# Kernel optimization log

Hardware: AMD Instinct MI355X
Metric: run time of the kernel (lower is better)

Reference implementation:

```python
import jax, jax.numpy as jnp
import numpy as np

INPUT_DIM, HIDDEN_DIM, N_HEADS, N_AGENTS = 256, 512, 8, 64
BATCH, N_ENTITIES = 128, 256


def setup_inputs() -> dict:
    key = jax.random.key(0)
    ks = jax.random.split(key, 6)
    x = jax.random.normal(ks[0], (BATCH, N_ENTITIES, INPUT_DIM), dtype=jnp.float32)
    # encode: LeakyReLU -> Linear(input_dim, hidden_dim)
    W_enc = jax.random.normal(ks[1], (INPUT_DIM, HIDDEN_DIM), dtype=jnp.float32) * (1.0 / np.sqrt(INPUT_DIM))
    b_enc = jnp.zeros((HIDDEN_DIM,), dtype=jnp.float32)
    # per-head full hidden x hidden projections, stacked on head axis
    WQ = jax.random.normal(ks[2], (N_HEADS, HIDDEN_DIM, HIDDEN_DIM), dtype=jnp.float32)
    WK = jax.random.normal(ks[3], (N_HEADS, HIDDEN_DIM, HIDDEN_DIM), dtype=jnp.float32)
    WV = jax.random.normal(ks[4], (N_HEADS, HIDDEN_DIM, HIDDEN_DIM), dtype=jnp.float32)
    return {"x": x, "W_enc": W_enc, "b_enc": b_enc, "WQ": WQ, "WK": WK, "WV": WV, "n_agents": N_AGENTS}


def reference(x, W_enc, b_enc, WQ, WK, WV, n_agents):
    scale = 1.0 / np.sqrt(WQ.shape[-1]).astype(np.float32)
    # encode: LeakyReLU(0.01) then Linear
    h = jax.nn.leaky_relu(x, negative_slope=0.01) @ W_enc + b_enc  # [b, e, H]
    ha = h[:, :n_agents]  # [b, a, H]
    # all heads at once: n = head axis
    Q = jnp.einsum('bah,nhd->nbad', ha, WQ)
    K = jnp.einsum('beh,nhd->nbed', h, WK)
    V = jnp.einsum('beh,nhd->nbed', h, WV)
    scores = jnp.einsum('nbad,nbed->nbae', Q, K) * scale
    p = jax.nn.softmax(scores, axis=-1)
    # redundant renormalization from the original code
    prob = p / (jnp.sum(p, axis=-1, keepdims=True) + 1e-12)
    z = jnp.einsum('nbae,nbed->nbad', prob, V)  # [n, b, a, H]
    return jnp.mean(z, axis=0)  # [b, a, H]
```

## Files before the change

kernel.cpp:

```cpp
#include <hip/hip_runtime.h>
#include <math.h>

#define BATCH  128
#define NENT   256
#define INDIM  256
#define HID    512
#define NHEAD  8
#define NAGENT 64
#define SCALE  0.04419417382415922f


typedef unsigned short u16;
typedef unsigned int   u32;

typedef __bf16 bf16x8  __attribute__((ext_vector_type(8)));
typedef float  floatx4 __attribute__((ext_vector_type(4)));
typedef u32    u32x4   __attribute__((ext_vector_type(4)));
typedef u32    u32x2   __attribute__((ext_vector_type(2)));

union Frag {
    u32x4 s;
    struct { u32x2 lo, hi; } p;
    bf16x8 v;
};

__device__ __forceinline__ u16 f2bf(float x) {
    u32 u = __float_as_uint(x);
    return (u16)((u + 0x7FFFu + ((u >> 16) & 1u)) >> 16);
}
__device__ __forceinline__ float bf2f(u16 b) {
    return __uint_as_float(((u32)b) << 16);
}
__device__ __forceinline__ void split4(const float4& r, ushort4& hh, ushort4& hl) {
    hh.x = f2bf(r.x); hl.x = f2bf(r.x - bf2f(hh.x));
    hh.y = f2bf(r.y); hl.y = f2bf(r.y - bf2f(hh.y));
    hh.z = f2bf(r.z); hl.z = f2bf(r.z - bf2f(hh.z));
    hh.w = f2bf(r.w); hl.w = f2bf(r.w - bf2f(hh.w));
}

__global__ __launch_bounds__(256) void wenc_t_kernel(const float* __restrict__ W,
                                                     u16* __restrict__ Wt_p) {
    __shared__ float tile[64][68];
    const int bid = blockIdx.x;
    const int k0 = (bid & 3) * 64;
    const int d0 = (bid >> 2) * 64;
    const int t = threadIdx.x;
    const int ki = t >> 2, dc = (t & 3) * 16;
    #pragma unroll
    for (int c = 0; c < 4; ++c)
        *(float4*)&tile[ki][dc + c * 4] =
            *(const float4*)(W + (size_t)(k0 + ki) * HID + d0 + dc + c * 4);
    __syncthreads();
    const int dr = t >> 2, kc = (t & 3) * 16;
    #pragma unroll
    for (int c = 0; c < 4; ++c) {
        float4 v = make_float4(tile[kc + c * 4 + 0][dr], tile[kc + c * 4 + 1][dr],
                               tile[kc + c * 4 + 2][dr], tile[kc + c * 4 + 3][dr]);
        ushort4 hh, hl; split4(v, hh, hl);
        const int kk = k0 + kc + c * 4;
        size_t o = (size_t)(d0 + dr) * 512 + (size_t)(kk >> 5) * 64 + (kk & 31);
        *(ushort4*)(Wt_p + o) = hh;
        *(ushort4*)(Wt_p + o + 32) = hl;
    }
}

__global__ __launch_bounds__(256) void enc_kernel(const float* __restrict__ x,
                                                  const u16* __restrict__ Wt_p,
                                                  const float* __restrict__ bias,
                                                  u16* __restrict__ h_p) {
    __shared__ u16 Ah[32][264];
    __shared__ u16 Al[32][264];
    const int r0 = blockIdx.x * 32;
    const int t  = threadIdx.x;
    {
        const int row = t >> 3;
        const float* xr = x + (size_t)(r0 + row) * INDIM;
        #pragma unroll
        for (int j = 0; j < 8; ++j) {
            const int k0 = ((t & 7) + j * 8) * 4;
            float4 v = *(const float4*)(xr + k0);
            v.x = v.x > 0.f ? v.x : 0.01f * v.x;
            v.y = v.y > 0.f ? v.y : 0.01f * v.y;
            v.z = v.z > 0.f ? v.z : 0.01f * v.z;
            v.w = v.w > 0.f ? v.w : 0.01f * v.w;
            ushort4 hh, hl; split4(v, hh, hl);
            *(ushort4*)&Ah[row][k0] = hh;
            *(ushort4*)&Al[row][k0] = hl;
        }
    }
    __syncthreads();

    const int wid = t >> 6, lane = t & 63, l15 = lane & 15, quad = lane >> 4;
    const int mbase = (wid & 1) * 16;
    const int nbase = (wid >> 1) * 256;
    const floatx4 z4 = {0.f, 0.f, 0.f, 0.f};
    floatx4 acc[16];
    #pragma unroll
    for (int i = 0; i < 16; ++i) acc[i] = z4;

    for (int ks = 0; ks < 8; ++ks) {
        const int k = ks * 32 + quad * 8;
        Frag Afh, Afl;
        Afh.s = *(const u32x4*)&Ah[mbase + l15][k];
        Afl.s = *(const u32x4*)&Al[mbase + l15][k];
        #pragma unroll
        for (int nt = 0; nt < 16; ++nt) {
            const int d = nbase + nt * 16 + l15;
            const size_t wo = (size_t)d * 512 + (size_t)ks * 64 + quad * 8;
            Frag Bh, Bl;
            Bh.s = *(const u32x4*)(Wt_p + wo);
            Bl.s = *(const u32x4*)(Wt_p + wo + 32);
            floatx4 c = acc[nt];
            c = __builtin_amdgcn_mfma_f32_16x16x32_bf16(Afh.v, Bh.v, c, 0, 0, 0);
            c = __builtin_amdgcn_mfma_f32_16x16x32_bf16(Afh.v, Bl.v, c, 0, 0, 0);
            c = __builtin_amdgcn_mfma_f32_16x16x32_bf16(Afl.v, Bh.v, c, 0, 0, 0);
            acc[nt] = c;
        }
    }
    #pragma unroll
    for (int nt = 0; nt < 16; ++nt) {
        const int d = nbase + nt * 16 + l15;
        const float bv = bias[d];
        #pragma unroll
        for (int r = 0; r < 4; ++r) {
            const float v = acc[nt][r] + bv;
            const u16 hi = f2bf(v);
            const u16 lo = f2bf(v - bf2f(hi));
            const size_t o = (size_t)(r0 + mbase + quad * 4 + r) * 1024
                           + (size_t)(d >> 5) * 64 + (d & 31);
            h_p[o]      = hi;
            h_p[o + 32] = lo;
        }
    }
}

__global__ __launch_bounds__(256) void ht_kernel(const u16* __restrict__ h_p,
                                                 u16* __restrict__ hT) {
    __shared__ u16 tile[64][72];
    const int bid = blockIdx.x;
    const int dt = bid & 7;
    const int et = (bid >> 3) & 3;
    const int b  = bid >> 5;
    const int t  = threadIdx.x;
    const int r  = t >> 2, cs = (t & 3) * 16;
    const int dg = dt * 64 + cs;
    const u16* src = h_p + (size_t)(b * 256 + et * 64 + r) * 1024
                   + (size_t)(dg >> 5) * 64 + (dg & 31);
    *(ushort4*)&tile[r][cs + 0]  = *(const ushort4*)(src + 0);
    *(ushort4*)&tile[r][cs + 4]  = *(const ushort4*)(src + 4);
    *(ushort4*)&tile[r][cs + 8]  = *(const ushort4*)(src + 8);
    *(ushort4*)&tile[r][cs + 12] = *(const ushort4*)(src + 12);
    __syncthreads();
    const int d = t >> 2, es = (t & 3) * 16;
    u16* dst = hT + (size_t)b * 131072 + (size_t)(dt * 64 + d) * 256 + et * 64 + es;
    #pragma unroll
    for (int c = 0; c < 4; ++c) {
        ushort4 v = make_ushort4(tile[es + c * 4 + 0][d], tile[es + c * 4 + 1][d],
                                 tile[es + c * 4 + 2][d], tile[es + c * 4 + 3][d]);
        *(ushort4*)(dst + c * 4) = v;
    }
}

__global__ __launch_bounds__(256) void wqk_kernel(const float* __restrict__ WQ,
                                                  const float* __restrict__ WK,
                                                  u16* __restrict__ Mt_p) {
    __shared__ u16 Ah[64][72], Al[64][72], Bh[64][72], Bl[64][72];
    const int bid = blockIdx.x;
    const int jt = (bid & 7) * 64;
    const int it = ((bid >> 3) & 7) * 64;
    const int n  = bid >> 6;
    const float* qp = WQ + (size_t)n * 262144;
    const float* kp = WK + (size_t)n * 262144;
    const int t = threadIdx.x;
    const int wid = t >> 6, lane = t & 63, l15 = lane & 15, quad = lane >> 4;
    const int srow = t >> 2, sc = (t & 3) * 16;

    const floatx4 z4 = {0.f, 0.f, 0.f, 0.f};
    floatx4 acc[4];
    #pragma unroll
    for (int i = 0; i < 4; ++i) acc[i] = z4;

    for (int kc = 0; kc < HID; kc += 64) {
        #pragma unroll
        for (int f = 0; f < 4; ++f) {
            float4 va = *(const float4*)(kp + (size_t)(jt + srow) * HID + kc + sc + f * 4);
            ushort4 hh, hl; split4(va, hh, hl);
            *(ushort4*)&Ah[srow][sc + f * 4] = hh;
            *(ushort4*)&Al[srow][sc + f * 4] = hl;
            float4 vb = *(const float4*)(qp + (size_t)(it + srow) * HID + kc + sc + f * 4);
            split4(vb, hh, hl);
            *(ushort4*)&Bh[srow][sc + f * 4] = hh;
            *(ushort4*)&Bl[srow][sc + f * 4] = hl;
        }
        __syncthreads();
        #pragma unroll
        for (int ks = 0; ks < 2; ++ks) {
            const int k = ks * 32 + quad * 8;
            Frag Afh, Afl;
            Afh.s = *(const u32x4*)&Ah[wid * 16 + l15][k];
            Afl.s = *(const u32x4*)&Al[wid * 16 + l15][k];
            #pragma unroll
            for (int nt = 0; nt < 4; ++nt) {
                Frag Bfh, Bfl;
                Bfh.s = *(const u32x4*)&Bh[nt * 16 + l15][k];
                Bfl.s = *(const u32x4*)&Bl[nt * 16 + l15][k];
                floatx4 c = acc[nt];
                c = __builtin_amdgcn_mfma_f32_16x16x32_bf16(Afh.v, Bfh.v, c, 0, 0, 0);
                c = __builtin_amdgcn_mfma_f32_16x16x32_bf16(Afh.v, Bfl.v, c, 0, 0, 0);
                c = __builtin_amdgcn_mfma_f32_16x16x32_bf16(Afl.v, Bfh.v, c, 0, 0, 0);
                acc[nt] = c;
            }
        }
        __syncthreads();
    }
    #pragma unroll
    for (int nt = 0; nt < 4; ++nt)
        #pragma unroll
        for (int r = 0; r < 4; ++r) {
            const float v = acc[nt][r] * SCALE;
            const u16 hi = f2bf(v);
            const u16 lo = f2bf(v - bf2f(hi));
            const int j = jt + wid * 16 + quad * 4 + r;
            const int i = it + nt * 16 + l15;
            const size_t o = (size_t)n * 524288 + (size_t)j * 1024
                           + (size_t)(i >> 5) * 64 + (i & 31);
            Mt_p[o]      = hi;
            Mt_p[o + 32] = lo;
        }
}

__global__ __launch_bounds__(256) void wvt_kernel(const float* __restrict__ WV,
                                                  u16* __restrict__ WVt) {
    __shared__ float tile[64][68];
    const int bid = blockIdx.x;
    const int i0 = (bid & 7) * 64;
    const int o0 = ((bid >> 3) & 7) * 64;
    const int n  = bid >> 6;
    const float* src = WV + (size_t)n * 262144;
    const int t  = threadIdx.x;
    const int di = t >> 2;
    const int dc = (t & 3) * 16;
    #pragma unroll
    for (int c = 0; c < 4; ++c)
        *(float4*)&tile[di][dc + c * 4] =
            *(const float4*)(src + (size_t)(i0 + di) * HID + o0 + dc + c * 4);
    __syncthreads();
    const int dr = t >> 2;
    const int ic = (t & 3) * 16;
    size_t o = (size_t)n * 262144 + (size_t)(o0 + dr) * HID + i0 + ic;
    #pragma unroll
    for (int c = 0; c < 4; ++c) {
        ushort4 v = make_ushort4(f2bf(tile[ic + c * 4 + 0][dr]), f2bf(tile[ic + c * 4 + 1][dr]),
                                 f2bf(tile[ic + c * 4 + 2][dr]), f2bf(tile[ic + c * 4 + 3][dr]));
        *(ushort4*)(WVt + o + c * 4) = v;
    }
}

template<bool USE_HT>
__global__ __launch_bounds__(256, 3) void attn_kernel(const u16* __restrict__ h_p,
                                                      const u16* __restrict__ Mt_p,
                                                      const u16* __restrict__ WVt,
                                                      const u16* __restrict__ hT,
                                                      float* __restrict__ out) {
    constexpr int SMSZ = USE_HT ? 34816 : 53504;
    __shared__ __align__(16) char SM[SMSZ];
    u16*   Th  = (u16*)SM;
    u16*   Tl  = (u16*)(SM + 16640);
    float* S   = (float*)SM;
    float* red = (float*)(SM + 33792);
    u16*   HbT = (u16*)SM;
    u16*   U   = (u16*)SM;
    u16*   Pt  = (u16*)(SM + (USE_HT ? 0 : 36864));

    const int bid = blockIdx.x;
    const int x7 = bid & 7;
    const int s  = bid >> 3;
    const int at = s & 1;
    const int n  = (x7 >> 1) | (((s >> 1) & 1) << 2);
    const int b  = ((s >> 2) << 1) | (x7 & 1);

    const int tid  = threadIdx.x;
    const int wid  = tid >> 6;
    const int lane = tid & 63;
    const int l15  = lane & 15;
    const int quad = lane >> 4;

    const u16* Mtp = Mt_p + (size_t)n * 524288;
    const u16* Wv  = WVt  + (size_t)n * 262144;
    const u16* hTb = hT + (size_t)b * 131072;
    const size_t hb_base = (size_t)b * 262144;
    const size_t ha_row0 = hb_base + (size_t)(at * 32) * 1024;

    const floatx4 z4 = {0.f, 0.f, 0.f, 0.f};
    floatx4 Sacc[8];
    #pragma unroll
    for (int i = 0; i < 8; ++i) Sacc[i] = z4;

    for (int H = 0; H < 2; ++H) {
        floatx4 Tacc[8];
        #pragma unroll
        for (int i = 0; i < 8; ++i) Tacc[i] = z4;
        for (int ks = 0; ks < 16; ++ks) {
            const int ko = ks * 64 + quad * 8;
            Frag Ahf[2], Alf[2];
            #pragma unroll
            for (int mt = 0; mt < 2; ++mt) {
                const size_t ro = ha_row0 + (size_t)(mt * 16 + l15) * 1024 + ko;
                Ahf[mt].s = *(const u32x4*)(h_p + ro);
                Alf[mt].s = *(const u32x4*)(h_p + ro + 32);
            }
            #pragma unroll
            for (int nt = 0; nt < 4; ++nt) {
                const int d = H * 256 + (wid * 4 + nt) * 16 + l15;
                const size_t mo = (size_t)d * 1024 + ko;
                Frag Bh, Bl;
                Bh.s = *(const u32x4*)(Mtp + mo);
                Bl.s = *(const u32x4*)(Mtp + mo + 32);
                #pragma unroll
                for (int mt = 0; mt < 2; ++mt) {
                    floatx4 c = Tacc[mt * 4 + nt];
                    c = __builtin_amdgcn_mfma_f32_16x16x32_bf16(Ahf[mt].v, Bh.v, c, 0, 0, 0);
                    c = __builtin_amdgcn_mfma_f32_16x16x32_bf16(Ahf[mt].v, Bl.v, c, 0, 0, 0);
                    c = __builtin_amdgcn_mfma_f32_16x16x32_bf16(Alf[mt].v, Bh.v, c, 0, 0, 0);
                    Tacc[mt * 4 + nt] = c;
                }
            }
        }
        __syncthreads();
        #pragma unroll
        for (int mt = 0; mt < 2; ++mt)
            #pragma unroll
            for (int nt = 0; nt < 4; ++nt)
                #pragma unroll
                for (int r = 0; r < 4; ++r) {
                    const float v = Tacc[mt * 4 + nt][r];
                    const int a  = mt * 16 + quad * 4 + r;
                    const int dl = (wid * 4 + nt) * 16 + l15;
                    const u16 hi = f2bf(v);
                    Th[a * 260 + dl] = hi;
                    Tl[a * 260 + dl] = f2bf(v - bf2f(hi));
                }
        __syncthreads();
        for (int ks = 0; ks < 8; ++ks) {
            const int kl = ks * 32 + quad * 8;
            const int ko = (H * 8 + ks) * 64 + quad * 8;
            Frag Ahf[4], Alf[4];
            #pragma unroll
            for (int mt = 0; mt < 4; ++mt) {
                const size_t ro = hb_base + (size_t)((wid * 4 + mt) * 16 + l15) * 1024 + ko;
                Ahf[mt].s = *(const u32x4*)(h_p + ro);
                Alf[mt].s = *(const u32x4*)(h_p + ro + 32);
            }
            #pragma unroll
            for (int nt = 0; nt < 2; ++nt) {
                const int ac = nt * 16 + l15;
                Frag Bfh, Bfl;
                Bfh.p.lo = *(const u32x2*)(Th + ac * 260 + kl);
                Bfh.p.hi = *(const u32x2*)(Th + ac * 260 + kl + 4);
                Bfl.p.lo = *(const u32x2*)(Tl + ac * 260 + kl);
                Bfl.p.hi = *(const u32x2*)(Tl + ac * 260 + kl + 4);
                #pragma unroll
                for (int mt = 0; mt < 4; ++mt) {
                    floatx4 c = Sacc[mt * 2 + nt];
                    c = __builtin_amdgcn_mfma_f32_16x16x32_bf16(Ahf[mt].v, Bfh.v, c, 0, 0, 0);
                    c = __builtin_amdgcn_mfma_f32_16x16x32_bf16(Ahf[mt].v, Bfl.v, c, 0, 0, 0);
                    c = __builtin_amdgcn_mfma_f32_16x16x32_bf16(Alf[mt].v, Bfh.v, c, 0, 0, 0);
                    Sacc[mt * 2 + nt] = c;
                }
            }
        }
    }
    __syncthreads();
    #pragma unroll
    for (int mt = 0; mt < 4; ++mt)
        #pragma unroll
        for (int nt = 0; nt < 2; ++nt)
            #pragma unroll
            for (int r = 0; r < 4; ++r) {
                const int e = (wid * 4 + mt) * 16 + quad * 4 + r;
                const int a = nt * 16 + l15;
                S[e * 33 + a] = Sacc[mt * 2 + nt][r];
            }
    __syncthreads();
    {
        const int a   = tid & 31;
        const int seg = tid >> 5;
        float v[32];
        #pragma unroll
        for (int i = 0; i < 32; ++i) v[i] = S[(seg * 32 + i) * 33 + a];
        float mx = v[0];
        #pragma unroll
        for (int i = 1; i < 32; ++i) mx = fmaxf(mx, v[i]);
        red[a * 8 + seg] = mx;
        __syncthreads();
        float gmx = red[a * 8 + 0];
        #pragma unroll
        for (int i = 1; i < 8; ++i) gmx = fmaxf(gmx, red[a * 8 + i]);
        __syncthreads();
        float sum = 0.f;
        #pragma unroll
        for (int i = 0; i < 32; ++i) { v[i] = expf(v[i] - gmx); sum += v[i]; }
        red[a * 8 + seg] = sum;
        __syncthreads();
        float tot = 0.f;
        #pragma unroll
        for (int i = 0; i < 8; ++i) tot += red[a * 8 + i];
        const float inv = 1.0f / tot;
        #pragma unroll
        for (int i = 0; i < 32; ++i)
            Pt[a * 260 + seg * 32 + i] = f2bf(v[i] * inv);
    }
    __syncthreads();
    floatx4 Uacc[16];
    #pragma unroll
    for (int i = 0; i < 16; ++i) Uacc[i] = z4;
    const int d0w = wid * 128;
    if (USE_HT) {
        for (int ep = 0; ep < 4; ++ep) {
            Frag Bc[2][8];
            #pragma unroll
            for (int sb = 0; sb < 2; ++sb)
                #pragma unroll
                for (int dt = 0; dt < 8; ++dt) {
                    const int d = d0w + dt * 16 + l15;
                    Bc[sb][dt].s = *(const u32x4*)(hTb + (size_t)d * 256
                                                   + (2 * ep + sb) * 32 + quad * 8);
                }
            #pragma unroll
            for (int sb = 0; sb < 2; ++sb) {
                const int et = 2 * ep + sb;
                Frag Ap[2];
                #pragma unroll
                for (int mt = 0; mt < 2; ++mt) {
                    const int ar = mt * 16 + l15;
                    Ap[mt].p.lo = *(const u32x2*)(Pt + ar * 260 + et * 32 + quad * 8);
                    Ap[mt].p.hi = *(const u32x2*)(Pt + ar * 260 + et * 32 + quad * 8 + 4);
                }
                #pragma unroll
                for (int dt = 0; dt < 8; ++dt)
                    #pragma unroll
                    for (int mt = 0; mt < 2; ++mt)
                        Uacc[mt * 8 + dt] = __builtin_amdgcn_mfma_f32_16x16x32_bf16(
                            Ap[mt].v, Bc[sb][dt].v, Uacc[mt * 8 + dt], 0, 0, 0);
            }
        }
    } else {
        u32* Hb32 = (u32*)HbT;
        for (int et = 0; et < 8; ++et) {
            {
                const int epi = lane & 15;
                const int q   = lane >> 4;
                const size_t r0p = hb_base + (size_t)(et * 32 + 2 * epi) * 1024;
                #pragma unroll
                for (int c = 0; c < 4; ++c) {
                    const int d0 = d0w + c * 32 + q * 8;
                    const size_t po = (size_t)(d0 >> 5) * 64 + (d0 & 31);
                    u32x4 u0 = *(const u32x4*)(h_p + r0p + po);
                    u32x4 u1 = *(const u32x4*)(h_p + r0p + 1024 + po);
                    #pragma unroll
                    for (int p = 0; p < 4; ++p) {
                        const u32 w0 = (u0[p] & 0xFFFFu) | (u1[p] << 16);
                        const u32 w1 = (u0[p] >> 16) | (u1[p] & 0xFFFF0000u);
                        Hb32[(d0 + 2 * p) * 18 + epi]     = w0;
                        Hb32[(d0 + 2 * p + 1) * 18 + epi] = w1;
                    }
                }
            }
            Frag Ap[2];
            #pragma unroll
            for (int mt = 0; mt < 2; ++mt) {
                const int ar = mt * 16 + l15;
                Ap[mt].p.lo = *(const u32x2*)(Pt + ar * 260 + et * 32 + quad * 8);
                Ap[mt].p.hi = *(const u32x2*)(Pt + ar * 260 + et * 32 + quad * 8 + 4);
            }
            #pragma unroll
            for (int dt = 0; dt < 8; ++dt) {
                const int d = d0w + dt * 16 + l15;
                Frag Bf;
                Bf.p.lo = *(const u32x2*)(HbT + d * 36 + quad * 8);
                Bf.p.hi = *(const u32x2*)(HbT + d * 36 + quad * 8 + 4);
                #pragma unroll
                for (int mt = 0; mt < 2; ++mt)
                    Uacc[mt * 8 + dt] = __builtin_amdgcn_mfma_f32_16x16x32_bf16(
                        Ap[mt].v, Bf.v, Uacc[mt * 8 + dt], 0, 0, 0);
            }
        }
    }
    __syncthreads();
    #pragma unroll
    for (int mt = 0; mt < 2; ++mt)
        #pragma unroll
        for (int dt = 0; dt < 8; ++dt)
            #pragma unroll
            for (int r = 0; r < 4; ++r) {
                const int a = mt * 16 + quad * 4 + r;
                const int d = d0w + dt * 16 + l15;
                U[a * 520 + d] = f2bf(Uacc[mt * 8 + dt][r]);
            }
    __syncthreads();
    floatx4 Zacc[16];
    #pragma unroll
    for (int i = 0; i < 16; ++i) Zacc[i] = z4;
    for (int kp = 0; kp < 8; ++kp) {
        Frag Bw[2][8];
        #pragma unroll
        for (int sb = 0; sb < 2; ++sb) {
            const int k = (kp * 2 + sb) * 32 + quad * 8;
            #pragma unroll
            for (int dt = 0; dt < 8; ++dt) {
                const int dn = (wid * 8 + dt) * 16 + l15;
                Bw[sb][dt].s = *(const u32x4*)(Wv + (size_t)dn * HID + k);
            }
        }
        #pragma unroll
        for (int sb = 0; sb < 2; ++sb) {
            const int k = (kp * 2 + sb) * 32 + quad * 8;
            Frag Au[2];
            #pragma unroll
            for (int mt = 0; mt < 2; ++mt) {
                Au[mt].p.lo = *(const u32x2*)(U + (mt * 16 + l15) * 520 + k);
                Au[mt].p.hi = *(const u32x2*)(U + (mt * 16 + l15) * 520 + k + 4);
            }
            #pragma unroll
            for (int dt = 0; dt < 8; ++dt)
                #pragma unroll
                for (int mt = 0; mt < 2; ++mt)
                    Zacc[mt * 8 + dt] = __builtin_amdgcn_mfma_f32_16x16x32_bf16(
                        Au[mt].v, Bw[sb][dt].v, Zacc[mt * 8 + dt], 0, 0, 0);
        }
    }
    float* ob = out + ((size_t)b * NAGENT + at * 32) * HID;
    #pragma unroll
    for (int mt = 0; mt < 2; ++mt)
        #pragma unroll
        for (int dt = 0; dt < 8; ++dt)
            #pragma unroll
            for (int r = 0; r < 4; ++r) {
                const int a  = mt * 16 + quad * 4 + r;
                const int dn = (wid * 8 + dt) * 16 + l15;
                atomicAdd(ob + (size_t)a * HID + dn, Zacc[mt * 8 + dt][r] * 0.125f);
            }
}

extern "C" void kernel_launch(void* const* d_in, const int* in_sizes, int n_in,
                              void* d_out, int out_size, void* d_ws, size_t ws_size,
                              hipStream_t stream) {
    const float* x     = (const float*)d_in[0];
    const float* W_enc = (const float*)d_in[1];
    const float* b_enc = (const float*)d_in[2];
    const float* WQ    = (const float*)d_in[3];
    const float* WK    = (const float*)d_in[4];
    const float* WV    = (const float*)d_in[5];
    float* out = (float*)d_out;

    char* ws = (char*)d_ws;
    u16* h_p  = (u16*)ws;
    u16* Mt_p = (u16*)(ws + 67108864);
    u16* WVt  = (u16*)(ws + 75497472);
    u16* hT   = (u16*)(ws + 79691776);
    u16* Wt_p = WVt;

    const bool useHT = ws_size >= (size_t)113246208;

    hipMemsetAsync(d_out, 0, (size_t)out_size * sizeof(float), stream);
    wenc_t_kernel<<<32, 256, 0, stream>>>(W_enc, Wt_p);
    enc_kernel<<<1024, 256, 0, stream>>>(x, Wt_p, b_enc, h_p);
    if (useHT) ht_kernel<<<4096, 256, 0, stream>>>(h_p, hT);
    wvt_kernel<<<512, 256, 0, stream>>>(WV, WVt);
    wqk_kernel<<<512, 256, 0, stream>>>(WQ, WK, Mt_p);
    if (useHT)
        attn_kernel<true><<<2048, 256, 0, stream>>>(h_p, Mt_p, WVt, hT, out);
    else
        attn_kernel<false><<<2048, 256, 0, stream>>>(h_p, Mt_p, WVt, hT, out);
}
```

Baseline: 971.0 us.

## Double-buffer global operand loads in register across all fused GEMM phases

Each GEMM stage of the fused attention kernel (T=ha·M, S=h·T, U=P·hT, Z=U·WV) now uses two register fragment sets. The loads for the next k-step are issued before the MFMAs of the current step, and the first loads of each stage are hoisted above the preceding __syncthreads. The goal is to hide global-memory latency behind matrix-core work instead of stalling at the start of each k-iteration. The cost is many more live VGPRs, which risks spills or lower occupancy. The prefetch loops also read one step past the last k-slice, into memory that is never used.

After: 961.4 us. About the same (-1.0%).

```diff
diff --git a/kernel.cpp b/kernel.cpp
--- a/kernel.cpp
+++ b/kernel.cpp
@@ -36,6 +36,9 @@
     hh.y = f2bf(r.y); hl.y = f2bf(r.y - bf2f(hh.y));
     hh.z = f2bf(r.z); hl.z = f2bf(r.z - bf2f(hh.z));
     hh.w = f2bf(r.w); hl.w = f2bf(r.w - bf2f(hh.w));
+}
+__device__ __forceinline__ floatx4 mm(const Frag& a, const Frag& b, floatx4 c) {
+    return __builtin_amdgcn_mfma_f32_16x16x32_bf16(a.v, b.v, c, 0, 0, 0);
 }
 
 __global__ __launch_bounds__(256) void wenc_t_kernel(const float* __restrict__ W,
@@ -296,36 +299,67 @@
     #pragma unroll
     for (int i = 0; i < 8; ++i) Sacc[i] = z4;
 
+    const u16* hA  = h_p + ha_row0 + (size_t)l15 * 1024 + quad * 8;
+    const u16* hB  = h_p + hb_base + (size_t)(wid * 64 + l15) * 1024 + quad * 8;
+
+#define LDA4(SET, KS) do { const u16* _p = hA + (size_t)(KS) * 64;                     \
+        SET##h0.s = *(const u32x4*)(_p);         SET##l0.s = *(const u32x4*)(_p + 32);   \
+        SET##h1.s = *(const u32x4*)(_p + 16384); SET##l1.s = *(const u32x4*)(_p + 16416);} while (0)
+#define LDB2(SET, KS, NT) do { const u16* _p = MtB + (NT) * 16384 + (size_t)(KS) * 64;  \
+        SET##h.s = *(const u32x4*)(_p);          SET##l.s = *(const u32x4*)(_p + 32); } while (0)
+#define MFA(AS, BS, NT) do {                                                            \
+        floatx4 c0 = Tacc[NT], c1 = Tacc[4 + (NT)];                                     \
+        c0 = mm(AS##h0, BS##h, c0); c0 = mm(AS##h0, BS##l, c0); c0 = mm(AS##l0, BS##h, c0); \
+        c1 = mm(AS##h1, BS##h, c1); c1 = mm(AS##h1, BS##l, c1); c1 = mm(AS##l1, BS##h, c1); \
+        Tacc[NT] = c0; Tacc[4 + (NT)] = c1; } while (0)
+#define LDP8(SET, KO) do { const u16* _p = hB + (size_t)(KO) * 64;                      \
+        SET##h0.s = *(const u32x4*)(_p);         SET##l0.s = *(const u32x4*)(_p + 32);   \
+        SET##h1.s = *(const u32x4*)(_p + 16384); SET##l1.s = *(const u32x4*)(_p + 16416);\
+        SET##h2.s = *(const u32x4*)(_p + 32768); SET##l2.s = *(const u32x4*)(_p + 32800);\
+        SET##h3.s = *(const u32x4*)(_p + 49152); SET##l3.s = *(const u32x4*)(_p + 49184);} while (0)
+#define MFMB(AS, KS) do {                                                               \
+        const int _kl = (KS) * 32 + quad * 8;                                           \
+        Frag _h0, _l0, _h1, _l1;                                                        \
+        _h0.p.lo = *(const u32x2*)(Th + l15 * 260 + _kl);                               \
+        _h0.p.hi = *(const u32x2*)(Th + l15 * 260 + _kl + 4);                           \
+        _l0.p.lo = *(const u32x2*)(Tl + l15 * 260 + _kl);                               \
+        _l0.p.hi = *(const u32x2*)(Tl + l15 * 260 + _kl + 4);                           \
+        _h1.p.lo = *(const u32x2*)(Th + (16 + l15) * 260 + _kl);                        \
+        _h1.p.hi = *(const u32x2*)(Th + (16 + l15) * 260 + _kl + 4);                    \
+        _l1.p.lo = *(const u32x2*)(Tl + (16 + l15) * 260 + _kl);                        \
+        _l1.p.hi = *(const u32x2*)(Tl + (16 + l15) * 260 + _kl + 4);                    \
+        Sacc[0] = mm(AS##h0, _h0, Sacc[0]); Sacc[0] = mm(AS##h0, _l0, Sacc[0]); Sacc[0] = mm(AS##l0, _h0, Sacc[0]); \
+        Sacc[2] = mm(AS##h1, _h0, Sacc[2]); Sacc[2] = mm(AS##h1, _l0, Sacc[2]); Sacc[2] = mm(AS##l1, _h0, Sacc[2]); \
+        Sacc[4] = mm(AS##h2, _h0, Sacc[4]); Sacc[4] = mm(AS##h2, _l0, Sacc[4]); Sacc[4] = mm(AS##l2, _h0, Sacc[4]); \
+        Sacc[6] = mm(AS##h3, _h0, Sacc[6]); Sacc[6] = mm(AS##h3, _l0, Sacc[6]); Sacc[6] = mm(AS##l3, _h0, Sacc[6]); \
+        Sacc[1] = mm(AS##h0, _h1, Sacc[1]); Sacc[1] = mm(AS##h0, _l1, Sacc[1]); Sacc[1] = mm(AS##l0, _h1, Sacc[1]); \
+        Sacc[3] = mm(AS##h1, _h1, Sacc[3]); Sacc[3] = mm(AS##h1, _l1, Sacc[3]); Sacc[3] = mm(AS##l1, _h1, Sacc[3]); \
+        Sacc[5] = mm(AS##h2, _h1, Sacc[5]); Sacc[5] = mm(AS##h2, _l1, Sacc[5]); Sacc[5] = mm(AS##l2, _h1, Sacc[5]); \
+        Sacc[7] = mm(AS##h3, _h1, Sacc[7]); Sacc[7] = mm(AS##h3, _l1, Sacc[7]); Sacc[7] = mm(AS##l3, _h1, Sacc[7]); } while (0)
+
     for (int H = 0; H < 2; ++H) {
         floatx4 Tacc[8];
         #pragma unroll
         for (int i = 0; i < 8; ++i) Tacc[i] = z4;
-        for (int ks = 0; ks < 16; ++ks) {
-            const int ko = ks * 64 + quad * 8;
-            Frag Ahf[2], Alf[2];
-            #pragma unroll
-            for (int mt = 0; mt < 2; ++mt) {
-                const size_t ro = ha_row0 + (size_t)(mt * 16 + l15) * 1024 + ko;
-                Ahf[mt].s = *(const u32x4*)(h_p + ro);
-                Alf[mt].s = *(const u32x4*)(h_p + ro + 32);
-            }
-            #pragma unroll
-            for (int nt = 0; nt < 4; ++nt) {
-                const int d = H * 256 + (wid * 4 + nt) * 16 + l15;
-                const size_t mo = (size_t)d * 1024 + ko;
-                Frag Bh, Bl;
-                Bh.s = *(const u32x4*)(Mtp + mo);
-                Bl.s = *(const u32x4*)(Mtp + mo + 32);
-                #pragma unroll
-                for (int mt = 0; mt < 2; ++mt) {
-                    floatx4 c = Tacc[mt * 4 + nt];
-                    c = __builtin_amdgcn_mfma_f32_16x16x32_bf16(Ahf[mt].v, Bh.v, c, 0, 0, 0);
-                    c = __builtin_amdgcn_mfma_f32_16x16x32_bf16(Ahf[mt].v, Bl.v, c, 0, 0, 0);
-                    c = __builtin_amdgcn_mfma_f32_16x16x32_bf16(Alf[mt].v, Bh.v, c, 0, 0, 0);
-                    Tacc[mt * 4 + nt] = c;
-                }
-            }
-        }
+        const u16* MtB = Mtp + (size_t)(H * 256 + wid * 64 + l15) * 1024 + quad * 8;
+        Frag A0h0, A0l0, A0h1, A0l1, A1h0, A1l0, A1h1, A1l1;
+        Frag B0h, B0l, B1h, B1l;
+        LDA4(A0, 0); LDB2(B0, 0, 0);
+        for (int ks = 0; ks < 16; ks += 2) {
+            LDA4(A1, ks + 1);
+            LDB2(B1, ks, 1);      MFA(A0, B0, 0);
+            LDB2(B0, ks, 2);      MFA(A0, B1, 1);
+            LDB2(B1, ks, 3);      MFA(A0, B0, 2);
+            LDB2(B0, ks + 1, 0);  MFA(A0, B1, 3);
+            LDA4(A0, ks + 2);
+            LDB2(B1, ks + 1, 1);  MFA(A1, B0, 0);
+            LDB2(B0, ks + 1, 2);  MFA(A1, B1, 1);
+            LDB2(B1, ks + 1, 3);  MFA(A1, B0, 2);
+            LDB2(B0, ks + 2, 0);  MFA(A1, B1, 3);
+        }
+        Frag P0h0, P0l0, P0h1, P0l1, P0h2, P0l2, P0h3, P0l3;
+        Frag P1h0, P1l0, P1h1, P1l1, P1h2, P1l2, P1h3, P1l3;
+        LDP8(P0, H * 8);
         __syncthreads();
         #pragma unroll
         for (int mt = 0; mt < 2; ++mt)
@@ -341,33 +375,11 @@
                     Tl[a * 260 + dl] = f2bf(v - bf2f(hi));
                 }
         __syncthreads();
-        for (int ks = 0; ks < 8; ++ks) {
-            const int kl = ks * 32 + quad * 8;
-            const int ko = (H * 8 + ks) * 64 + quad * 8;
-            Frag Ahf[4], Alf[4];
-            #pragma unroll
-            for (int mt = 0; mt < 4; ++mt) {
-                const size_t ro = hb_base + (size_t)((wid * 4 + mt) * 16 + l15) * 1024 + ko;
-                Ahf[mt].s = *(const u32x4*)(h_p + ro);
-                Alf[mt].s = *(const u32x4*)(h_p + ro + 32);
-            }
-            #pragma unroll
-            for (int nt = 0; nt < 2; ++nt) {
-                const int ac = nt * 16 + l15;
-                Frag Bfh, Bfl;
-                Bfh.p.lo = *(const u32x2*)(Th + ac * 260 + kl);
-                Bfh.p.hi = *(const u32x2*)(Th + ac * 260 + kl + 4);
-                Bfl.p.lo = *(const u32x2*)(Tl + ac * 260 + kl);
-                Bfl.p.hi = *(const u32x2*)(Tl + ac * 260 + kl + 4);
-                #pragma unroll
-                for (int mt = 0; mt < 4; ++mt) {
-                    floatx4 c = Sacc[mt * 2 + nt];
-                    c = __builtin_amdgcn_mfma_f32_16x16x32_bf16(Ahf[mt].v, Bfh.v, c, 0, 0, 0);
-                    c = __builtin_amdgcn_mfma_f32_16x16x32_bf16(Ahf[mt].v, Bfl.v, c, 0, 0, 0);
-                    c = __builtin_amdgcn_mfma_f32_16x16x32_bf16(Alf[mt].v, Bfh.v, c, 0, 0, 0);
-                    Sacc[mt * 2 + nt] = c;
-                }
-            }
+        for (int ks = 0; ks < 8; ks += 2) {
+            LDP8(P1, H * 8 + ks + 1);
+            MFMB(P0, ks);
+            LDP8(P0, H * 8 + ks + 2);
+            MFMB(P1, ks + 1);
         }
     }
     __syncthreads();
@@ -410,41 +422,45 @@
         for (int i = 0; i < 32; ++i)
             Pt[a * 260 + seg * 32 + i] = f2bf(v[i] * inv);
     }
-    __syncthreads();
     floatx4 Uacc[16];
     #pragma unroll
     for (int i = 0; i < 16; ++i) Uacc[i] = z4;
     const int d0w = wid * 128;
     if (USE_HT) {
-        for (int ep = 0; ep < 4; ++ep) {
-            Frag Bc[2][8];
-            #pragma unroll
-            for (int sb = 0; sb < 2; ++sb)
-                #pragma unroll
-                for (int dt = 0; dt < 8; ++dt) {
-                    const int d = d0w + dt * 16 + l15;
-                    Bc[sb][dt].s = *(const u32x4*)(hTb + (size_t)d * 256
-                                                   + (2 * ep + sb) * 32 + quad * 8);
-                }
-            #pragma unroll
-            for (int sb = 0; sb < 2; ++sb) {
-                const int et = 2 * ep + sb;
-                Frag Ap[2];
-                #pragma unroll
-                for (int mt = 0; mt < 2; ++mt) {
-                    const int ar = mt * 16 + l15;
-                    Ap[mt].p.lo = *(const u32x2*)(Pt + ar * 260 + et * 32 + quad * 8);
-                    Ap[mt].p.hi = *(const u32x2*)(Pt + ar * 260 + et * 32 + quad * 8 + 4);
-                }
-                #pragma unroll
-                for (int dt = 0; dt < 8; ++dt)
-                    #pragma unroll
-                    for (int mt = 0; mt < 2; ++mt)
-                        Uacc[mt * 8 + dt] = __builtin_amdgcn_mfma_f32_16x16x32_bf16(
-                            Ap[mt].v, Bc[sb][dt].v, Uacc[mt * 8 + dt], 0, 0, 0);
-            }
-        }
+        const u16* hTB = hTb + (size_t)(d0w + l15) * 256 + quad * 8;
+#define LDC8(SET, ET) do { const u16* _p = hTB + (size_t)(ET) * 32;                     \
+        SET##b0.s = *(const u32x4*)(_p);         SET##b1.s = *(const u32x4*)(_p + 4096); \
+        SET##b2.s = *(const u32x4*)(_p + 8192);  SET##b3.s = *(const u32x4*)(_p + 12288);\
+        SET##b4.s = *(const u32x4*)(_p + 16384); SET##b5.s = *(const u32x4*)(_p + 20480);\
+        SET##b6.s = *(const u32x4*)(_p + 24576); SET##b7.s = *(const u32x4*)(_p + 28672);} while (0)
+#define MFMC(SET, ET) do {                                                              \
+        Frag _a0, _a1;                                                                  \
+        _a0.p.lo = *(const u32x2*)(Pt + l15 * 260 + (ET) * 32 + quad * 8);              \
+        _a0.p.hi = *(const u32x2*)(Pt + l15 * 260 + (ET) * 32 + quad * 8 + 4);          \
+        _a1.p.lo = *(const u32x2*)(Pt + (16 + l15) * 260 + (ET) * 32 + quad * 8);       \
+        _a1.p.hi = *(const u32x2*)(Pt + (16 + l15) * 260 + (ET) * 32 + quad * 8 + 4);   \
+        Uacc[0] = mm(_a0, SET##b0, Uacc[0]);  Uacc[8]  = mm(_a1, SET##b0, Uacc[8]);     \
+        Uacc[1] = mm(_a0, SET##b1, Uacc[1]);  Uacc[9]  = mm(_a1, SET##b1, Uacc[9]);     \
+        Uacc[2] = mm(_a0, SET##b2, Uacc[2]);  Uacc[10] = mm(_a1, SET##b2, Uacc[10]);    \
+        Uacc[3] = mm(_a0, SET##b3, Uacc[3]);  Uacc[11] = mm(_a1, SET##b3, Uacc[11]);    \
+        Uacc[4] = mm(_a0, SET##b4, Uacc[4]);  Uacc[12] = mm(_a1, SET##b4, Uacc[12]);    \
+        Uacc[5] = mm(_a0, SET##b5, Uacc[5]);  Uacc[13] = mm(_a1, SET##b5, Uacc[13]);    \
+        Uacc[6] = mm(_a0, SET##b6, Uacc[6]);  Uacc[14] = mm(_a1, SET##b6, Uacc[14]);    \
+        Uacc[7] = mm(_a0, SET##b7, Uacc[7]);  Uacc[15] = mm(_a1, SET##b7, Uacc[15]); } while (0)
+        Frag C0b0, C0b1, C0b2, C0b3, C0b4, C0b5, C0b6, C0b7;
+        Frag C1b0, C1b1, C1b2, C1b3, C1b4, C1b5, C1b6, C1b7;
+        LDC8(C0, 0);
+        __syncthreads();
+        for (int et = 0; et < 8; et += 2) {
+            LDC8(C1, et + 1);
+            MFMC(C0, et);
+            LDC8(C0, et + 2);
+            MFMC(C1, et + 1);
+        }
+#undef LDC8
+#undef MFMC
     } else {
+        __syncthreads();
         u32* Hb32 = (u32*)HbT;
         for (int et = 0; et < 8; ++et) {
             {
@@ -497,38 +513,46 @@
                 const int d = d0w + dt * 16 + l15;
                 U[a * 520 + d] = f2bf(Uacc[mt * 8 + dt][r]);
             }
-    __syncthreads();
     floatx4 Zacc[16];
     #pragma unroll
     for (int i = 0; i < 16; ++i) Zacc[i] = z4;
-    for (int kp = 0; kp < 8; ++kp) {
-        Frag Bw[2][8];
-        #pragma unroll
-        for (int sb = 0; sb < 2; ++sb) {
-            const int k = (kp * 2 + sb) * 32 + quad * 8;
-            #pragma unroll
-            for (int dt = 0; dt < 8; ++dt) {
-                const int dn = (wid * 8 + dt) * 16 + l15;
-                Bw[sb][dt].s = *(const u32x4*)(Wv + (size_t)dn * HID + k);
-            }
-        }
-        #pragma unroll
-        for (int sb = 0; sb < 2; ++sb) {
-            const int k = (kp * 2 + sb) * 32 + quad * 8;
-            Frag Au[2];
-            #pragma unroll
-            for (int mt = 0; mt < 2; ++mt) {
-                Au[mt].p.lo = *(const u32x2*)(U + (mt * 16 + l15) * 520 + k);
-                Au[mt].p.hi = *(const u32x2*)(U + (mt * 16 + l15) * 520 + k + 4);
-            }
-            #pragma unroll
-            for (int dt = 0; dt < 8; ++dt)
-                #pragma unroll
-                for (int mt = 0; mt < 2; ++mt)
-                    Zacc[mt * 8 + dt] = __builtin_amdgcn_mfma_f32_16x16x32_bf16(
-                        Au[mt].v, Bw[sb][dt].v, Zacc[mt * 8 + dt], 0, 0, 0);
-        }
-    }
+    const u16* WvB = Wv + (size_t)(wid * 128 + l15) * 512 + quad * 8;
+#define LDD8(SET, KS) do { const u16* _p = WvB + (size_t)(KS) * 32;                     \
+        SET##b0.s = *(const u32x4*)(_p);         SET##b1.s = *(const u32x4*)(_p + 8192); \
+        SET##b2.s = *(const u32x4*)(_p + 16384); SET##b3.s = *(const u32x4*)(_p + 24576);\
+        SET##b4.s = *(const u32x4*)(_p + 32768); SET##b5.s = *(const u32x4*)(_p + 40960);\
+        SET##b6.s = *(const u32x4*)(_p + 49152); SET##b7.s = *(const u32x4*)(_p + 57344);} while (0)
+#define MFMD(SET, KS) do {                                                              \
+        Frag _a0, _a1;                                                                  \
+        _a0.p.lo = *(const u32x2*)(U + l15 * 520 + (KS) * 32 + quad * 8);               \
+        _a0.p.hi = *(const u32x2*)(U + l15 * 520 + (KS) * 32 + quad * 8 + 4);           \
+        _a1.p.lo = *(const u32x2*)(U + (16 + l15) * 520 + (KS) * 32 + quad * 8);        \
+        _a1.p.hi = *(const u32x2*)(U + (16 + l15) * 520 + (KS) * 32 + quad * 8 + 4);    \
+        Zacc[0] = mm(_a0, SET##b0, Zacc[0]);  Zacc[8]  = mm(_a1, SET##b0, Zacc[8]);     \
+        Zacc[1] = mm(_a0, SET##b1, Zacc[1]);  Zacc[9]  = mm(_a1, SET##b1, Zacc[9]);     \
+        Zacc[2] = mm(_a0, SET##b2, Zacc[2]);  Zacc[10] = mm(_a1, SET##b2, Zacc[10]);    \
+        Zacc[3] = mm(_a0, SET##b3, Zacc[3]);  Zacc[11] = mm(_a1, SET##b3, Zacc[11]);    \
+        Zacc[4] = mm(_a0, SET##b4, Zacc[4]);  Zacc[12] = mm(_a1, SET##b4, Zacc[12]);    \
+        Zacc[5] = mm(_a0, SET##b5, Zacc[5]);  Zacc[13] = mm(_a1, SET##b5, Zacc[13]);    \
+        Zacc[6] = mm(_a0, SET##b6, Zacc[6]);  Zacc[14] = mm(_a1, SET##b6, Zacc[14]);    \
+        Zacc[7] = mm(_a0, SET##b7, Zacc[7]);  Zacc[15] = mm(_a1, SET##b7, Zacc[15]); } while (0)
+    Frag D0b0, D0b1, D0b2, D0b3, D0b4, D0b5, D0b6, D0b7;
+    Frag D1b0, D1b1, D1b2, D1b3, D1b4, D1b5, D1b6, D1b7;
+    LDD8(D0, 0);
+    __syncthreads();
+    for (int ks = 0; ks < 16; ks += 2) {
+        LDD8(D1, ks + 1);
+        MFMD(D0, ks);
+        LDD8(D0, ks + 2);
+        MFMD(D1, ks + 1);
+    }
+#undef LDD8
+#undef MFMD
+#undef LDA4
+#undef LDB2
+#undef MFA
+#undef LDP8
+#undef MFMB
     float* ob = out + ((size_t)b * NAGENT + at * 32) * HID;
     #pragma unroll
     for (int mt = 0; mt < 2; ++mt)
```

## Stage Mt and ha tiles through LDS with global_load_lds in attention T-phase

Applied to the files above, without the earlier changes.

The first GEMM phase (ha × Mt) of the attention kernel now copies each k-slice of Mt and of the agent rows of h into shared memory with the direct global-to-LDS load instruction. Fragments are then read from LDS instead of loading them straight from global memory. The goal is coalesced, shared global traffic for a tile that all waves reuse. It adds two block barriers per k-step with no double buffering, and it raises LDS use for the USE_HT variant, which may cut occupancy.

After: 894.5 us. -7.9%, faster.

```diff
diff --git a/kernel.cpp b/kernel.cpp
--- a/kernel.cpp
+++ b/kernel.cpp
@@ -36,6 +36,14 @@
     hh.y = f2bf(r.y); hl.y = f2bf(r.y - bf2f(hh.y));
     hh.z = f2bf(r.z); hl.z = f2bf(r.z - bf2f(hh.z));
     hh.w = f2bf(r.w); hl.w = f2bf(r.w - bf2f(hh.w));
+}
+__device__ __forceinline__ floatx4 mm(const Frag& a, const Frag& b, floatx4 c) {
+    return __builtin_amdgcn_mfma_f32_16x16x32_bf16(a.v, b.v, c, 0, 0, 0);
+}
+__device__ __forceinline__ void gl16(const u16* g, char* l) {
+    __builtin_amdgcn_global_load_lds(
+        (const __attribute__((address_space(1))) u32*)g,
+        (__attribute__((address_space(3))) u32*)l, 16, 0, 0);
 }
 
 __global__ __launch_bounds__(256) void wenc_t_kernel(const float* __restrict__ W,
@@ -262,12 +270,12 @@
                                                       const u16* __restrict__ WVt,
                                                       const u16* __restrict__ hT,
                                                       float* __restrict__ out) {
-    constexpr int SMSZ = USE_HT ? 34816 : 53504;
+    constexpr int SMSZ = USE_HT ? 37888 : 53504;
     __shared__ __align__(16) char SM[SMSZ];
     u16*   Th  = (u16*)SM;
     u16*   Tl  = (u16*)(SM + 16640);
     float* S   = (float*)SM;
-    float* red = (float*)(SM + 33792);
+    float* red = (float*)(SM + (USE_HT ? 36864 : 33792));
     u16*   HbT = (u16*)SM;
     u16*   U   = (u16*)SM;
     u16*   Pt  = (u16*)(SM + (USE_HT ? 0 : 36864));
@@ -297,36 +305,47 @@
     for (int i = 0; i < 8; ++i) Sacc[i] = z4;
 
     for (int H = 0; H < 2; ++H) {
+        __syncthreads();
         floatx4 Tacc[8];
         #pragma unroll
         for (int i = 0; i < 8; ++i) Tacc[i] = z4;
+        const int d0 = H * 256;
+        const u16* mtS = (const u16*)SM;
+        const u16* haS = (const u16*)(SM + 32768);
         for (int ks = 0; ks < 16; ++ks) {
-            const int ko = ks * 64 + quad * 8;
-            Frag Ahf[2], Alf[2];
-            #pragma unroll
-            for (int mt = 0; mt < 2; ++mt) {
-                const size_t ro = ha_row0 + (size_t)(mt * 16 + l15) * 1024 + ko;
-                Ahf[mt].s = *(const u32x4*)(h_p + ro);
-                Alf[mt].s = *(const u32x4*)(h_p + ro + 32);
-            }
+            #pragma unroll
+            for (int j = 0; j < 8; ++j) {
+                const int i = wid * 8 + j;
+                const int chunk = i >> 2;
+                const int row   = (i & 3) * 64 + lane;
+                gl16(Mtp + (size_t)(d0 + row) * 1024 + ks * 64 + chunk * 8,
+                     SM + i * 1024);
+            }
+            {
+                const int chunk = wid * 2 + (lane >> 5);
+                const int row   = lane & 31;
+                gl16(h_p + ha_row0 + (size_t)row * 1024 + ks * 64 + chunk * 8,
+                     SM + 32768 + wid * 1024);
+            }
+            __syncthreads();
+            Frag Ah0, Al0, Ah1, Al1;
+            Ah0.s = *(const u32x4*)(haS + ((quad)     * 32 + l15)      * 8);
+            Al0.s = *(const u32x4*)(haS + ((4 + quad) * 32 + l15)      * 8);
+            Ah1.s = *(const u32x4*)(haS + ((quad)     * 32 + 16 + l15) * 8);
+            Al1.s = *(const u32x4*)(haS + ((4 + quad) * 32 + 16 + l15) * 8);
             #pragma unroll
             for (int nt = 0; nt < 4; ++nt) {
-                const int d = H * 256 + (wid * 4 + nt) * 16 + l15;
-                const size_t mo = (size_t)d * 1024 + ko;
+                const int row = (wid * 4 + nt) * 16 + l15;
                 Frag Bh, Bl;
-                Bh.s = *(const u32x4*)(Mtp + mo);
-                Bl.s = *(const u32x4*)(Mtp + mo + 32);
-                #pragma unroll
-                for (int mt = 0; mt < 2; ++mt) {
-                    floatx4 c = Tacc[mt * 4 + nt];
-                    c = __builtin_amdgcn_mfma_f32_16x16x32_bf16(Ahf[mt].v, Bh.v, c, 0, 0, 0);
-                    c = __builtin_amdgcn_mfma_f32_16x16x32_bf16(Ahf[mt].v, Bl.v, c, 0, 0, 0);
-                    c = __builtin_amdgcn_mfma_f32_16x16x32_bf16(Alf[mt].v, Bh.v, c, 0, 0, 0);
-                    Tacc[mt * 4 + nt] = c;
-                }
-            }
-        }
-        __syncthreads();
+                Bh.s = *(const u32x4*)(mtS + ((quad)     * 256 + row) * 8);
+                Bl.s = *(const u32x4*)(mtS + ((4 + quad) * 256 + row) * 8);
+                floatx4 c0 = Tacc[nt], c1 = Tacc[4 + nt];
+                c0 = mm(Ah0, Bh, c0); c0 = mm(Ah0, Bl, c0); c0 = mm(Al0, Bh, c0);
+                c1 = mm(Ah1, Bh, c1); c1 = mm(Ah1, Bl, c1); c1 = mm(Al1, Bh, c1);
+                Tacc[nt] = c0; Tacc[4 + nt] = c1;
+            }
+            __syncthreads();
+        }
         #pragma unroll
         for (int mt = 0; mt < 2; ++mt)
             #pragma unroll
@@ -453,16 +472,16 @@
                 const size_t r0p = hb_base + (size_t)(et * 32 + 2 * epi) * 1024;
                 #pragma unroll
                 for (int c = 0; c < 4; ++c) {
-                    const int d0 = d0w + c * 32 + q * 8;
-                    const size_t po = (size_t)(d0 >> 5) * 64 + (d0 & 31);
+                    const int d0c = d0w + c * 32 + q * 8;
+                    const size_t po = (size_t)(d0c >> 5) * 64 + (d0c & 31);
                     u32x4 u0 = *(const u32x4*)(h_p + r0p + po);
                     u32x4 u1 = *(const u32x4*)(h_p + r0p + 1024 + po);
                     #pragma unroll
                     for (int p = 0; p < 4; ++p) {
                         const u32 w0 = (u0[p] & 0xFFFFu) | (u1[p] << 16);
                         const u32 w1 = (u0[p] >> 16) | (u1[p] & 0xFFFF0000u);
-                        Hb32[(d0 + 2 * p) * 18 + epi]     = w0;
-                        Hb32[(d0 + 2 * p + 1) * 18 + epi] = w1;
+                        Hb32[(d0c + 2 * p) * 18 + epi]     = w0;
+                        Hb32[(d0c + 2 * p + 1) * 18 + epi] = w1;
                     }
                 }
             }
```
